# Kernel tuning notes

Measured on AMD Instinct MI355X. Metric: run time of the kernel, lower is better.

## Reference

```python
import jax, jax.numpy as jnp
import numpy as np

N, E, FIN, H, G, L = 100000, 300000, 128, 256, 4000, 5
BN_EPS = 1e-5

def setup_inputs() -> dict:
    key = jax.random.key(0)
    ks = jax.random.split(key, 24)
    s = 0.05
    inp = {
        "x": jax.random.normal(ks[0], (N, FIN), dtype=jnp.float32),
        "edge_index": jax.random.randint(ks[1], (2, E), 0, N, dtype=jnp.int64),
        "batch": jnp.sort(jax.random.randint(ks[2], (N,), 0, G, dtype=jnp.int64)),
        # input projection
        "in_W": jax.random.normal(ks[3], (FIN, H), dtype=jnp.float32) * s,
        "in_b": jnp.zeros((H,), dtype=jnp.float32),
        # stacked per-layer GIN MLP params (Linear-BN-ReLU-Linear-BN-ReLU)
        "conv_W1": jax.random.normal(ks[4], (L, H, H), dtype=jnp.float32) * s,
        "conv_b1": jnp.zeros((L, H), dtype=jnp.float32),
        "conv_g1": jnp.ones((L, H), dtype=jnp.float32),
        "conv_be1": jnp.zeros((L, H), dtype=jnp.float32),
        "conv_W2": jax.random.normal(ks[5], (L, H, H), dtype=jnp.float32) * s,
        "conv_b2": jnp.zeros((L, H), dtype=jnp.float32),
        "conv_g2": jnp.ones((L, H), dtype=jnp.float32),
        "conv_be2": jnp.zeros((L, H), dtype=jnp.float32),
        "eps": jnp.zeros((L,), dtype=jnp.float32),
        # head MLP
        "head_W1": jax.random.normal(ks[6], (H, H // 2), dtype=jnp.float32) * s,
        "head_b1": jnp.zeros((H // 2,), dtype=jnp.float32),
        "head_W2": jax.random.normal(ks[7], (H // 2, 1), dtype=jnp.float32) * s,
        "head_b2": jnp.zeros((1,), dtype=jnp.float32),
    }
    return inp

def _bn(h, g, b):
    # BatchNorm1d over node dim (training-mode batch stats)
    m = jnp.mean(h, axis=0)
    v = jnp.var(h, axis=0)
    return g * (h - m) * jax.lax.rsqrt(v + BN_EPS) + b

def reference(x, edge_index, batch, in_W, in_b, conv_W1, conv_b1, conv_g1,
              conv_be1, conv_W2, conv_b2, conv_g2, conv_be2, eps,
              head_W1, head_b1, head_W2, head_b2):
    src, dst = edge_index[0], edge_index[1]
    h = jax.nn.relu(x @ in_W + in_b)  # [N,H]
    for l in range(L):
        agg = jax.ops.segment_sum(h[src], dst, num_segments=N)  # scatter-add
        z = (1.0 + eps[l]) * h + agg
        z = jax.nn.relu(_bn(z @ conv_W1[l] + conv_b1[l], conv_g1[l], conv_be1[l]))
        h = jax.nn.relu(_bn(z @ conv_W2[l] + conv_b2[l], conv_g2[l], conv_be2[l]))
        # dropout is identity in eval/reference
    # global mean pool by graph id
    sums = jax.ops.segment_sum(h, batch, num_segments=G)  # [G,H]
    cnt = jax.ops.segment_sum(jnp.ones((N,), h.dtype), batch, num_segments=G)
    pooled = sums / jnp.maximum(cnt, 1.0)[:, None]
    hid = jax.nn.relu(pooled @ head_W1 + head_b1)
    return hid @ head_W2 + head_b2  # [G,1]
```

## Files before the change

### kernel.cpp

```cpp
#include <hip/hip_runtime.h>
#include <hip/hip_bf16.h>
#include <stdint.h>
#include <stddef.h>

#define NN 100000
#define NE 300000
#define FINDIM 128
#define HD 256
#define NG 4000
#define NLAYER 5
#define MPAD 100096
#define NT (MPAD/32)
#define MG 384

typedef __attribute__((ext_vector_type(8))) short bf8;
typedef __attribute__((ext_vector_type(4))) float f4;

__device__ __forceinline__ unsigned short f2bf(float f){
  union { float f; unsigned u; } uf; uf.f = f;
  unsigned r = uf.u + 0x7fffu + ((uf.u >> 16) & 1u);
  return (unsigned short)(r >> 16);
}
__device__ __forceinline__ float bf2f(unsigned short h){
  union { unsigned u; float f; } uf; uf.u = ((unsigned)h) << 16; return uf.f;
}

__device__ __forceinline__ void gload16(const void* g, void* l){
  __builtin_amdgcn_global_load_lds((const __attribute__((address_space(1))) void*)g,
                                   (__attribute__((address_space(3))) void*)l, 16, 0, 0);
}

__global__ void k_zero(int* __restrict__ p, int n){
  int i = blockIdx.x*256 + threadIdx.x;
  if(i < n) p[i] = 0;
}

__global__ void k_count(const int* __restrict__ ei, int* __restrict__ counts){
  int e = blockIdx.x*256 + threadIdx.x;
  if(e < NE) atomicAdd(&counts[ei[NE + e]], 1);
}

__global__ void k_scan_partial(const int* __restrict__ counts, int* __restrict__ partials){
  __shared__ int sw[4];
  int b = blockIdx.x, t = threadIdx.x;
  int base = b*1024 + t*4;
  int s = 0;
  #pragma unroll
  for(int j=0;j<4;j++){ int i = base+j; if(i < NN) s += counts[i]; }
  #pragma unroll
  for(int d=1; d<64; d<<=1) s += __shfl_xor(s, d, 64);
  if((t & 63) == 0) sw[t>>6] = s;
  __syncthreads();
  if(t == 0) partials[b] = sw[0]+sw[1]+sw[2]+sw[3];
}

__global__ void k_scan_tot(int* __restrict__ partials, int* __restrict__ offsets, int nb){
  __shared__ int sm[128];
  int t = threadIdx.x;
  int v = (t < nb) ? partials[t] : 0;
  sm[t] = v; __syncthreads();
  for(int d=1; d<128; d<<=1){
    int x = 0;
    if(t >= d) x = sm[t-d];
    __syncthreads();
    sm[t] += x;
    __syncthreads();
  }
  if(t < nb) partials[t] = sm[t] - v;
  if(t == 127) offsets[NN] = sm[127];
}

__global__ void k_scan_final(const int* __restrict__ counts, const int* __restrict__ partials,
                             int* __restrict__ offsets, int* __restrict__ cursor){
  __shared__ int wsum[4];
  int b = blockIdx.x, t = threadIdx.x;
  int base = b*1024 + t*4;
  int c[4]; int ts = 0;
  #pragma unroll
  for(int j=0;j<4;j++){ int i = base+j; c[j] = (i < NN) ? counts[i] : 0; ts += c[j]; }
  int lane = t & 63;
  int inc = ts;
  #pragma unroll
  for(int d=1; d<64; d<<=1){ int x = __shfl_up(inc, d, 64); if(lane >= d) inc += x; }
  if(lane == 63) wsum[t>>6] = inc;
  __syncthreads();
  int woff = 0;
  for(int w2=0; w2<(t>>6); w2++) woff += wsum[w2];
  int excl = partials[b] + woff + inc - ts;
  #pragma unroll
  for(int j=0;j<4;j++){
    int i = base+j;
    if(i < NN){ offsets[i] = excl; cursor[i] = excl; excl += c[j]; }
  }
}

__global__ void k_fill(const int* __restrict__ ei, int* __restrict__ cursor, int* __restrict__ eidx){
  int e = blockIdx.x*256 + threadIdx.x;
  if(e < NE){
    int d = ei[NE + e];
    int pos = atomicAdd(&cursor[d], 1);
    eidx[pos] = ei[e];
  }
}

__global__ void k_wt(const float* __restrict__ src, unsigned short* __restrict__ dst, int K, int Ncols){
  int l = blockIdx.y;
  size_t base = (size_t)l * K * Ncols;
  int i = blockIdx.x*256 + threadIdx.x;
  if(i < K*Ncols){
    int k = i / Ncols, n = i % Ncols;
    dst[base + (size_t)n*K + k] = f2bf(src[base + i]);
  }
}

template<int TRANS, bool RELUOUT, bool STATS>
__global__ __launch_bounds__(256, 3) void k_gemmb(
    const unsigned short* __restrict__ A, const unsigned short* __restrict__ Bt,
    const float* __restrict__ bias, const float* __restrict__ preS,
    const float* __restrict__ preT, unsigned short* __restrict__ C,
    float* __restrict__ stats)
{
  __shared__ __align__(16) unsigned short As[2][8192];
  __shared__ __align__(16) unsigned short Cs[4][1152];
  __shared__ __align__(16) float SP[512];
  const int t = threadIdx.x;
  const int lane = t & 63, w = t >> 6;
  const int q = lane >> 4, ln = lane & 15;
  const int nh = blockIdx.x & 1;
  const int mg = blockIdx.x >> 1;
  const int nbase = nh*128 + w*32;

  if(TRANS){ SP[t] = preS[t]; SP[256 + t] = preT[t]; }

  bf8 bb[2][8];
  #pragma unroll
  for(int nf=0; nf<2; nf++)
    #pragma unroll
    for(int s=0; s<8; s++)
      bb[nf][s] = *(const bf8*)(Bt + (size_t)(nbase + nf*16 + ln)*HD + s*32 + q*8);

  float bv[2];
  #pragma unroll
  for(int nf=0; nf<2; nf++) bv[nf] = bias[nbase + nf*16 + ln];

  auto issueA = [&](int mt, int b){
    const int m0 = mt*32;
    #pragma unroll
    for(int j=0; j<4; j++){
      int slot = j*256 + t;
      int row = slot >> 5, p = slot & 31;
      int c = p ^ (row & 7);
      gload16(A + (size_t)(m0 + row)*HD + c*8, &As[b][(j*256 + w*64)*8]);
    }
  };

  float sacc[2] = {0.f, 0.f}, ssacc[2] = {0.f, 0.f};

  int mt = mg, tc = 0;
  if(mt < NT) issueA(mt, 0);
  for(; mt < NT; mt += MG, tc++){
    __syncthreads();
    int mtn = mt + MG;
    if(mtn < NT) issueA(mtn, (tc+1)&1);
    const unsigned short* Ab = As[tc&1];
    const int m0 = mt*32;
    const bool padt = (m0 >= NN);

    f4 acc[2][2];
    #pragma unroll
    for(int i=0;i<2;i++)
      #pragma unroll
      for(int j=0;j<2;j++) acc[i][j] = (f4){0.f,0.f,0.f,0.f};

    #pragma unroll
    for(int s=0; s<8; s++){
      bf8 af[2];
      #pragma unroll
      for(int mi=0; mi<2; mi++){
        int row = mi*16 + ln;
        int p = (s*4 + q) ^ (row & 7);
        af[mi] = *(const bf8*)&Ab[row*256 + p*8];
      }
      if(TRANS){
        f4 s0 = *(const f4*)&SP[s*32 + q*8];
        f4 s1 = *(const f4*)&SP[s*32 + q*8 + 4];
        f4 t0 = *(const f4*)&SP[256 + s*32 + q*8];
        f4 t1 = *(const f4*)&SP[256 + s*32 + q*8 + 4];
        float scv[8] = {s0.x,s0.y,s0.z,s0.w,s1.x,s1.y,s1.z,s1.w};
        float shv[8] = {t0.x,t0.y,t0.z,t0.w,t1.x,t1.y,t1.z,t1.w};
        #pragma unroll
        for(int mi=0; mi<2; mi++){
          #pragma unroll
          for(int j=0;j<8;j++){
            float v = bf2f((unsigned short)af[mi][j]);
            v = fmaxf(fmaf(scv[j], v, shv[j]), 0.f);
            af[mi][j] = (short)f2bf(v);
          }
        }
        if(padt){
          af[0] = (bf8){0,0,0,0,0,0,0,0};
          af[1] = (bf8){0,0,0,0,0,0,0,0};
        }
      }
      #pragma unroll
      for(int mi=0; mi<2; mi++)
        #pragma unroll
        for(int nf=0; nf<2; nf++)
          acc[mi][nf] = __builtin_amdgcn_mfma_f32_16x16x32_bf16(af[mi], bb[nf][s], acc[mi][nf], 0, 0, 0);
    }

    if(STATS){
      #pragma unroll
      for(int nf=0; nf<2; nf++)
        #pragma unroll
        for(int mi=0; mi<2; mi++)
          #pragma unroll
          for(int r=0; r<4; r++){
            float v = acc[mi][nf][r];
            sacc[nf] += v; ssacc[nf] = fmaf(v, v, ssacc[nf]);
          }
    }

    unsigned short* wsc = &Cs[w][0];
    #pragma unroll
    for(int mi=0; mi<2; mi++)
      #pragma unroll
      for(int nf=0; nf<2; nf++)
        #pragma unroll
        for(int r=0; r<4; r++){
          float v = acc[mi][nf][r] + bv[nf];
          if(RELUOUT) v = fmaxf(v, 0.f);
          if(padt) v = 0.f;
          wsc[(mi*16 + q*4 + r)*36 + nf*16 + ln] = f2bf(v);
        }
    int r2 = lane >> 1, ch = lane & 1;
    size_t cb = (size_t)(m0 + r2)*HD + nh*128 + w*32;
    uint4 u0 = *(const uint4*)&wsc[r2*36 + ch*8];
    uint4 u1 = *(const uint4*)&wsc[r2*36 + (ch+2)*8];
    *(uint4*)&C[cb + ch*8]     = u0;
    *(uint4*)&C[cb + (ch+2)*8] = u1;
  }

  if(STATS){
    #pragma unroll
    for(int nf=0; nf<2; nf++){
      float s = sacc[nf], ss = ssacc[nf];
      s  += __shfl_xor(s, 16, 64);  s  += __shfl_xor(s, 32, 64);
      ss += __shfl_xor(ss, 16, 64); ss += __shfl_xor(ss, 32, 64);
      if(q == 0){
        int gn = nbase + nf*16 + ln;
        atomicAdd(&stats[gn], s);
        atomicAdd(&stats[HD + gn], ss);
      }
    }
  }
}

__global__ __launch_bounds__(256, 3) void k_gemmb_in(
    const float* __restrict__ A, const unsigned short* __restrict__ Bt,
    const float* __restrict__ bias, unsigned short* __restrict__ C)
{
  __shared__ __align__(16) unsigned short As[4096];
  __shared__ __align__(16) unsigned short Cs[4][1152];
  const int t = threadIdx.x;
  const int lane = t & 63, w = t >> 6;
  const int q = lane >> 4, ln = lane & 15;
  const int nh = blockIdx.x & 1;
  const int mg = blockIdx.x >> 1;
  const int nbase = nh*128 + w*32;

  bf8 bb[2][4];
  #pragma unroll
  for(int nf=0; nf<2; nf++)
    #pragma unroll
    for(int s=0; s<4; s++)
      bb[nf][s] = *(const bf8*)(Bt + (size_t)(nbase + nf*16 + ln)*FINDIM + s*32 + q*8);

  float bv[2];
  #pragma unroll
  for(int nf=0; nf<2; nf++) bv[nf] = bias[nbase + nf*16 + ln];

  for(int mt = mg; mt < NT; mt += MG){
    const int m0 = mt*32;
    const bool padt = (m0 >= NN);
    __syncthreads();
    #pragma unroll
    for(int j=0; j<2; j++){
      int slot = j*256 + t;
      int row = slot >> 4, p = slot & 15;
      int c = p ^ (row & 7);
      int gm = m0 + row;
      f4 v0 = (f4){0.f,0.f,0.f,0.f}, v1 = (f4){0.f,0.f,0.f,0.f};
      if(gm < NN){
        v0 = *(const f4*)&A[(size_t)gm*FINDIM + c*8];
        v1 = *(const f4*)&A[(size_t)gm*FINDIM + c*8 + 4];
      }
      ushort4 a0, a1;
      a0.x = f2bf(v0.x); a0.y = f2bf(v0.y); a0.z = f2bf(v0.z); a0.w = f2bf(v0.w);
      a1.x = f2bf(v1.x); a1.y = f2bf(v1.y); a1.z = f2bf(v1.z); a1.w = f2bf(v1.w);
      *(ushort4*)&As[row*128 + p*8]     = a0;
      *(ushort4*)&As[row*128 + p*8 + 4] = a1;
    }
    __syncthreads();

    f4 acc[2][2];
    #pragma unroll
    for(int i=0;i<2;i++)
      #pragma unroll
      for(int j=0;j<2;j++) acc[i][j] = (f4){0.f,0.f,0.f,0.f};

    #pragma unroll
    for(int s=0; s<4; s++){
      bf8 af[2];
      #pragma unroll
      for(int mi=0; mi<2; mi++){
        int row = mi*16 + ln;
        int p = (s*4 + q) ^ (row & 7);
        af[mi] = *(const bf8*)&As[row*128 + p*8];
      }
      #pragma unroll
      for(int mi=0; mi<2; mi++)
        #pragma unroll
        for(int nf=0; nf<2; nf++)
          acc[mi][nf] = __builtin_amdgcn_mfma_f32_16x16x32_bf16(af[mi], bb[nf][s], acc[mi][nf], 0, 0, 0);
    }

    unsigned short* wsc = &Cs[w][0];
    #pragma unroll
    for(int mi=0; mi<2; mi++)
      #pragma unroll
      for(int nf=0; nf<2; nf++)
        #pragma unroll
        for(int r=0; r<4; r++){
          float v = fmaxf(acc[mi][nf][r] + bv[nf], 0.f);
          if(padt) v = 0.f;
          wsc[(mi*16 + q*4 + r)*36 + nf*16 + ln] = f2bf(v);
        }
    int r2 = lane >> 1, ch = lane & 1;
    size_t cb = (size_t)(m0 + r2)*HD + nh*128 + w*32;
    uint4 u0 = *(const uint4*)&wsc[r2*36 + ch*8];
    uint4 u1 = *(const uint4*)&wsc[r2*36 + (ch+2)*8];
    *(uint4*)&C[cb + ch*8]     = u0;
    *(uint4*)&C[cb + (ch+2)*8] = u1;
  }
}

__global__ void k_bnfin(const float* __restrict__ cs, const float* __restrict__ bias,
                        const float* __restrict__ g, const float* __restrict__ be,
                        float* __restrict__ sc, float* __restrict__ sh){
  int c = threadIdx.x;
  float m0 = cs[c] * (1.0f/NN);
  float mean = m0 + bias[c];
  float var  = cs[HD + c] * (1.0f/NN) - m0*m0;
  float s = g[c] * rsqrtf(var + 1e-5f);
  sc[c] = s;
  sh[c] = be[c] - mean*s;
}

__device__ __forceinline__ f4 act4(ushort4 uv, f4 s4, f4 t4, int ident){
  f4 u;
  u.x = bf2f(uv.x); u.y = bf2f(uv.y); u.z = bf2f(uv.z); u.w = bf2f(uv.w);
  if(!ident){
    u.x = fmaxf(fmaf(s4.x, u.x, t4.x), 0.f);
    u.y = fmaxf(fmaf(s4.y, u.y, t4.y), 0.f);
    u.z = fmaxf(fmaf(s4.z, u.z, t4.z), 0.f);
    u.w = fmaxf(fmaf(s4.w, u.w, t4.w), 0.f);
  }
  return u;
}

__global__ __launch_bounds__(256) void k_agg(const unsigned short* __restrict__ src,
    unsigned short* __restrict__ dst,
    const int* __restrict__ offs, const int* __restrict__ eidx,
    const float* __restrict__ eps, int l,
    const float* __restrict__ sc, const float* __restrict__ sh, int ident)
{
  int wv = threadIdx.x >> 6;
  int n = blockIdx.x*4 + wv;
  if(n >= NN) return;
  int lane = threadIdx.x & 63;
  int c = lane << 2;
  f4 s4 = (f4){0.f,0.f,0.f,0.f}, t4 = (f4){0.f,0.f,0.f,0.f};
  if(!ident){ s4 = *(const f4*)(sc + c); t4 = *(const f4*)(sh + c); }
  float ep = 1.f + eps[l];
  f4 a = act4(*(const ushort4*)(src + (size_t)n*HD + c), s4, t4, ident);
  f4 acc;
  acc.x = ep*a.x; acc.y = ep*a.y; acc.z = ep*a.z; acc.w = ep*a.w;
  int lo = offs[n], hi = offs[n+1];
  for(int base = lo; base < hi; base += 64){
    int rem = hi - base; if(rem > 64) rem = 64;
    int idx = 0;
    if(base + lane < hi) idx = eidx[base + lane];
    int j = 0;
    for(; j + 4 <= rem; j += 4){
      int s0 = __shfl(idx, j, 64),   s1 = __shfl(idx, j+1, 64);
      int s2 = __shfl(idx, j+2, 64), s3 = __shfl(idx, j+3, 64);
      ushort4 u0 = *(const ushort4*)(src + (size_t)s0*HD + c);
      ushort4 u1 = *(const ushort4*)(src + (size_t)s1*HD + c);
      ushort4 u2 = *(const ushort4*)(src + (size_t)s2*HD + c);
      ushort4 u3 = *(const ushort4*)(src + (size_t)s3*HD + c);
      f4 a0 = act4(u0, s4, t4, ident), a1 = act4(u1, s4, t4, ident);
      f4 a2 = act4(u2, s4, t4, ident), a3 = act4(u3, s4, t4, ident);
      acc.x += (a0.x + a1.x) + (a2.x + a3.x);
      acc.y += (a0.y + a1.y) + (a2.y + a3.y);
      acc.z += (a0.z + a1.z) + (a2.z + a3.z);
      acc.w += (a0.w + a1.w) + (a2.w + a3.w);
    }
    for(; j < rem; j++){
      int s0 = __shfl(idx, j, 64);
      f4 a0 = act4(*(const ushort4*)(src + (size_t)s0*HD + c), s4, t4, ident);
      acc.x += a0.x; acc.y += a0.y; acc.z += a0.z; acc.w += a0.w;
    }
  }
  ushort4 o;
  o.x = f2bf(acc.x); o.y = f2bf(acc.y); o.z = f2bf(acc.z); o.w = f2bf(acc.w);
  *(ushort4*)(dst + (size_t)n*HD + c) = o;
}

__device__ __forceinline__ int lowb(const int* __restrict__ arr, int n, int key){
  int lo = 0, hi = n;
  while(lo < hi){ int mid = (lo + hi) >> 1; if(arr[mid] < key) lo = mid + 1; else hi = mid; }
  return lo;
}

__global__ __launch_bounds__(256) void k_pool(const unsigned short* __restrict__ src,
    const int* __restrict__ batch,
    const float* __restrict__ sc, const float* __restrict__ sh, float* __restrict__ pooled)
{
  int wv = threadIdx.x >> 6;
  int g = blockIdx.x*4 + wv;
  if(g >= NG) return;
  int lane = threadIdx.x & 63;
  int c = lane << 2;
  int lo = lowb(batch, NN, g);
  int hi = lowb(batch, NN, g+1);
  f4 s4 = *(const f4*)(sc + c);
  f4 t4 = *(const f4*)(sh + c);
  f4 acc = (f4){0.f,0.f,0.f,0.f};
  for(int n=lo; n<hi; n++){
    ushort4 uv = *(const ushort4*)(src + (size_t)n*HD + c);
    acc.x += fmaxf(fmaf(s4.x, bf2f(uv.x), t4.x), 0.f);
    acc.y += fmaxf(fmaf(s4.y, bf2f(uv.y), t4.y), 0.f);
    acc.z += fmaxf(fmaf(s4.z, bf2f(uv.z), t4.z), 0.f);
    acc.w += fmaxf(fmaf(s4.w, bf2f(uv.w), t4.w), 0.f);
  }
  float inv = 1.0f / fmaxf((float)(hi - lo), 1.0f);
  acc.x *= inv; acc.y *= inv; acc.z *= inv; acc.w *= inv;
  *(f4*)(pooled + (size_t)g*HD + c) = acc;
}

__global__ __launch_bounds__(128) void k_head(const float* __restrict__ pooled,
    const float* __restrict__ W1, const float* __restrict__ b1,
    const float* __restrict__ W2, const float* __restrict__ b2, float* __restrict__ out)
{
  __shared__ float p[HD];
  __shared__ float red[2];
  int g = blockIdx.x, t = threadIdx.x;
  if(t < 64) *(f4*)&p[t*4] = *(const f4*)(pooled + (size_t)g*HD + t*4);
  __syncthreads();
  float s = b1[t];
  for(int k=0;k<HD;k++) s = fmaf(p[k], W1[k*128 + t], s);
  float o = fmaxf(s, 0.f) * W2[t];
  #pragma unroll
  for(int d=1; d<64; d<<=1) o += __shfl_xor(o, d, 64);
  if((t & 63) == 0) red[t>>6] = o;
  __syncthreads();
  if(t == 0) out[g] = red[0] + red[1] + b2[0];
}

extern "C" void kernel_launch(void* const* d_in, const int* in_sizes, int n_in,
                              void* d_out, int out_size, void* d_ws, size_t ws_size,
                              hipStream_t stream) {
  const float* x    = (const float*)d_in[0];
  const int*   ei   = (const int*)  d_in[1];
  const int*   bat  = (const int*)  d_in[2];
  const float* inW  = (const float*)d_in[3];
  const float* inb  = (const float*)d_in[4];
  const float* W1   = (const float*)d_in[5];
  const float* b1   = (const float*)d_in[6];
  const float* g1   = (const float*)d_in[7];
  const float* be1  = (const float*)d_in[8];
  const float* W2   = (const float*)d_in[9];
  const float* b2   = (const float*)d_in[10];
  const float* g2   = (const float*)d_in[11];
  const float* be2  = (const float*)d_in[12];
  const float* eps  = (const float*)d_in[13];
  const float* hW1  = (const float*)d_in[14];
  const float* hb1  = (const float*)d_in[15];
  const float* hW2  = (const float*)d_in[16];
  const float* hb2  = (const float*)d_in[17];
  float* out = (float*)d_out;

  char* p = (char*)d_ws;
  auto alloc = [&](size_t bytes)->char*{
    char* r = p; p += (bytes + 255) & ~(size_t)255; return r;
  };
  unsigned short* B0 = (unsigned short*)alloc((size_t)MPAD*HD*2);
  unsigned short* B1 = (unsigned short*)alloc((size_t)MPAD*HD*2);
  unsigned short* Wtin = (unsigned short*)alloc((size_t)FINDIM*HD*2);
  unsigned short* Wt1  = (unsigned short*)alloc((size_t)NLAYER*HD*HD*2);
  unsigned short* Wt2  = (unsigned short*)alloc((size_t)NLAYER*HD*HD*2);
  int* counts  = (int*)alloc((size_t)NN*4);
  int* offsets = (int*)alloc((size_t)(NN+1)*4);
  int* cursor  = (int*)alloc((size_t)NN*4);
  int* eidx    = (int*)alloc((size_t)NE*4);
  int* partials= (int*)alloc(128*4);
  float* cs    = (float*)alloc(4*HD*4);
  float* bnp   = (float*)alloc(4*HD*4);
  float* pooled= (float*)alloc((size_t)NG*HD*4);

  k_zero<<<(NN+255)/256, 256, 0, stream>>>(counts, NN);
  k_count<<<(NE+255)/256, 256, 0, stream>>>(ei, counts);
  int nb = (NN + 1023)/1024;
  k_scan_partial<<<nb, 256, 0, stream>>>(counts, partials);
  k_scan_tot<<<1, 128, 0, stream>>>(partials, offsets, nb);
  k_scan_final<<<nb, 256, 0, stream>>>(counts, partials, offsets, cursor);
  k_fill<<<(NE+255)/256, 256, 0, stream>>>(ei, cursor, eidx);

  k_wt<<<dim3((FINDIM*HD+255)/256, 1), 256, 0, stream>>>(inW, Wtin, FINDIM, HD);
  k_wt<<<dim3((HD*HD+255)/256, NLAYER), 256, 0, stream>>>(W1, Wt1, HD, HD);
  k_wt<<<dim3((HD*HD+255)/256, NLAYER), 256, 0, stream>>>(W2, Wt2, HD, HD);

  {
    int padInts = (MPAD - NN) * HD / 2;
    k_zero<<<(padInts+255)/256, 256, 0, stream>>>((int*)(B1 + (size_t)NN*HD), padInts);
  }

  k_gemmb_in<<<2*MG, 256, 0, stream>>>(x, Wtin, inb, B0);

  float* sc1 = bnp, *sh1 = bnp + HD, *sc2 = bnp + 2*HD, *sh2 = bnp + 3*HD;
  unsigned short* hbuf = B0;
  unsigned short* tbuf = B1;
  for(int l=0; l<NLAYER; l++){
    k_zero<<<4, 256, 0, stream>>>((int*)cs, 4*HD);
    k_agg<<<(NN+3)/4, 256, 0, stream>>>(hbuf, tbuf, offsets, eidx, eps, l, sc2, sh2, l==0 ? 1 : 0);
    k_gemmb<0, false, true><<<2*MG, 256, 0, stream>>>(tbuf, Wt1 + (size_t)l*HD*HD, b1 + l*HD,
                                                      nullptr, nullptr, hbuf, cs);
    k_bnfin<<<1, HD, 0, stream>>>(cs, b1 + l*HD, g1 + l*HD, be1 + l*HD, sc1, sh1);
    k_gemmb<1, false, true><<<2*MG, 256, 0, stream>>>(hbuf, Wt2 + (size_t)l*HD*HD, b2 + l*HD,
                                                      sc1, sh1, tbuf, cs + 2*HD);
    k_bnfin<<<1, HD, 0, stream>>>(cs + 2*HD, b2 + l*HD, g2 + l*HD, be2 + l*HD, sc2, sh2);
    unsigned short* tmp = hbuf; hbuf = tbuf; tbuf = tmp;
  }

  k_pool<<<(NG+3)/4, 256, 0, stream>>>(hbuf, bat, sc2, sh2, pooled);
  k_head<<<NG, 128, 0, stream>>>(pooled, hW1, hb1, hW2, hb2, out);
}
```

Before: 902.4 us.

## Prefetch two A tiles ahead with explicit vmcnt waits and apply BN transform in LDS

The GEMM main loop now issues the next two A tiles up front. It waits on explicit vmcnt counts instead of relying on __syncthreads, so global-to-LDS loads overlap more with compute. For the TRANS variant, the per-column BN scale/shift+ReLU is applied once per element in LDS before the MFMA loop, rather than in registers on every fragment load. This adds extra barriers and an LDS read-modify-write pass, and the hand-tuned waitcnt values must match the number of outstanding loads exactly.

```diff
diff --git a/kernel.cpp b/kernel.cpp
--- a/kernel.cpp
+++ b/kernel.cpp
@@ -15,6 +15,13 @@
 
 typedef __attribute__((ext_vector_type(8))) short bf8;
 typedef __attribute__((ext_vector_type(4))) float f4;
+
+#define FENCE() __asm__ volatile("" ::: "memory")
+#define WAITVM0() __asm__ volatile("s_waitcnt vmcnt(0)" ::: "memory")
+#define WAITVM4() __asm__ volatile("s_waitcnt vmcnt(4)" ::: "memory")
+#define WAITVM6() __asm__ volatile("s_waitcnt vmcnt(6)" ::: "memory")
+#define WAITLGKM() __asm__ volatile("s_waitcnt lgkmcnt(0)" ::: "memory")
+#define BARRIER() do { FENCE(); __builtin_amdgcn_s_barrier(); FENCE(); } while(0)
 
 __device__ __forceinline__ unsigned short f2bf(float f){
   union { float f; unsigned u; } uf; uf.f = f;
@@ -130,7 +137,7 @@
   const int mg = blockIdx.x >> 1;
   const int nbase = nh*128 + w*32;
 
-  if(TRANS){ SP[t] = preS[t]; SP[256 + t] = preT[t]; }
+  if(TRANS){ SP[t] = preS[t]; SP[256 + t] = preT[t]; WAITLGKM(); }
 
   bf8 bb[2][8];
   #pragma unroll
@@ -156,15 +163,50 @@
 
   float sacc[2] = {0.f, 0.f}, ssacc[2] = {0.f, 0.f};
 
-  int mt = mg, tc = 0;
-  if(mt < NT) issueA(mt, 0);
-  for(; mt < NT; mt += MG, tc++){
-    __syncthreads();
-    int mtn = mt + MG;
-    if(mtn < NT) issueA(mtn, (tc+1)&1);
-    const unsigned short* Ab = As[tc&1];
+  issueA(mg, 0);
+  issueA(mg + MG, 1);
+
+  int tc = 0;
+  for(int mt = mg; mt < NT; mt += MG, tc++){
+    const bool last = (mt + MG >= NT);
+    if(last)           WAITVM0();
+    else if(tc == 0)   WAITVM4();
+    else               WAITVM6();
+    BARRIER();
+
+    unsigned short* Ab = &As[tc&1][0];
     const int m0 = mt*32;
     const bool padt = (m0 >= NN);
+
+    if(TRANS){
+      #pragma unroll
+      for(int j=0; j<4; j++){
+        int slot = j*256 + t;
+        if(padt){
+          *(uint4*)&Ab[slot*8] = (uint4){0u,0u,0u,0u};
+        } else {
+          int row = slot >> 5, p = slot & 31;
+          int c = p ^ (row & 7);
+          uint4 u = *(const uint4*)&Ab[slot*8];
+          f4 s0 = *(const f4*)&SP[c*8];
+          f4 s1 = *(const f4*)&SP[c*8 + 4];
+          f4 t0 = *(const f4*)&SP[256 + c*8];
+          f4 t1 = *(const f4*)&SP[256 + c*8 + 4];
+          float scv[8] = {s0.x,s0.y,s0.z,s0.w,s1.x,s1.y,s1.z,s1.w};
+          float shv[8] = {t0.x,t0.y,t0.z,t0.w,t1.x,t1.y,t1.z,t1.w};
+          unsigned short* us = (unsigned short*)&u;
+          #pragma unroll
+          for(int e=0; e<8; e++){
+            float v = bf2f(us[e]);
+            v = fmaxf(fmaf(scv[e], v, shv[e]), 0.f);
+            us[e] = f2bf(v);
+          }
+          *(uint4*)&Ab[slot*8] = u;
+        }
+      }
+      WAITLGKM();
+      BARRIER();
+    }
 
     f4 acc[2][2];
     #pragma unroll
@@ -180,27 +222,6 @@
         int row = mi*16 + ln;
         int p = (s*4 + q) ^ (row & 7);
         af[mi] = *(const bf8*)&Ab[row*256 + p*8];
-      }
-      if(TRANS){
-        f4 s0 = *(const f4*)&SP[s*32 + q*8];
-        f4 s1 = *(const f4*)&SP[s*32 + q*8 + 4];
-        f4 t0 = *(const f4*)&SP[256 + s*32 + q*8];
-        f4 t1 = *(const f4*)&SP[256 + s*32 + q*8 + 4];
-        float scv[8] = {s0.x,s0.y,s0.z,s0.w,s1.x,s1.y,s1.z,s1.w};
-        float shv[8] = {t0.x,t0.y,t0.z,t0.w,t1.x,t1.y,t1.z,t1.w};
-        #pragma unroll
-        for(int mi=0; mi<2; mi++){
-          #pragma unroll
-          for(int j=0;j<8;j++){
-            float v = bf2f((unsigned short)af[mi][j]);
-            v = fmaxf(fmaf(scv[j], v, shv[j]), 0.f);
-            af[mi][j] = (short)f2bf(v);
-          }
-        }
-        if(padt){
-          af[0] = (bf8){0,0,0,0,0,0,0,0};
-          af[1] = (bf8){0,0,0,0,0,0,0,0};
-        }
       }
       #pragma unroll
       for(int mi=0; mi<2; mi++)
@@ -233,12 +254,18 @@
           if(padt) v = 0.f;
           wsc[(mi*16 + q*4 + r)*36 + nf*16 + ln] = f2bf(v);
         }
-    int r2 = lane >> 1, ch = lane & 1;
-    size_t cb = (size_t)(m0 + r2)*HD + nh*128 + w*32;
-    uint4 u0 = *(const uint4*)&wsc[r2*36 + ch*8];
-    uint4 u1 = *(const uint4*)&wsc[r2*36 + (ch+2)*8];
-    *(uint4*)&C[cb + ch*8]     = u0;
-    *(uint4*)&C[cb + (ch+2)*8] = u1;
+    {
+      int r2 = lane >> 1, ch = lane & 1;
+      size_t cb = (size_t)(m0 + r2)*HD + nh*128 + w*32;
+      uint4 u0 = *(const uint4*)&wsc[r2*36 + ch*8];
+      uint4 u1 = *(const uint4*)&wsc[r2*36 + (ch+2)*8];
+      *(uint4*)&C[cb + ch*8]     = u0;
+      *(uint4*)&C[cb + (ch+2)*8] = u1;
+    }
+
+    WAITLGKM();
+    BARRIER();
+    if(mt + 2*MG < NT) issueA(mt + 2*MG, tc&1);
   }
 
   if(STATS){
```

After: 840.5 us. -6.9%, faster.
